# Kernel tuning notes

Hardware: AMD Instinct MI355X
Metric: run time of the kernel (lower is better)

Reference implementation:

```python
import jax, jax.numpy as jnp
import numpy as np

NUM_EMBEDDINGS = 512
EMBEDDING_DIM = 64
COMMITMENT_COST = 0.25


def setup_inputs() -> dict:
    key = jax.random.key(0)
    k1, k2 = jax.random.split(key)
    inputs = jax.random.normal(k1, (4, 64, 32, 32, 32), dtype=jnp.float32)
    # torch init: uniform(-1/K, 1/K)
    lim = 1.0 / NUM_EMBEDDINGS
    embedding = jax.random.uniform(k2, (NUM_EMBEDDINGS, EMBEDDING_DIM),
                                   dtype=jnp.float32, minval=-lim, maxval=lim)
    return {"inputs": inputs, "embedding": embedding}


def reference(inputs, embedding):
    # inputs: [B, C, D, H, W] with C == embedding_dim
    x = jnp.transpose(inputs, (0, 2, 3, 4, 1))            # [B,D,H,W,C]
    input_shape = x.shape
    flat = x.reshape(-1, EMBEDDING_DIM)                    # [N,C]
    # squared euclidean distances via matmul expansion
    d = (jnp.sum(flat ** 2, axis=1, keepdims=True)
         + jnp.sum(embedding ** 2, axis=1)
         - 2.0 * flat @ embedding.T)                       # [N,K]
    encoding_indices = jnp.argmin(d, axis=1)               # [N]
    quantized = embedding[encoding_indices].reshape(input_shape)  # [B,D,H,W,C]
    q_latent_loss = jnp.mean((jax.lax.stop_gradient(quantized) - x) ** 2)
    e_latent_loss = jnp.mean((quantized - jax.lax.stop_gradient(x)) ** 2)
    loss = q_latent_loss + COMMITMENT_COST * e_latent_loss
    # straight-through estimator
    quantized = x + jax.lax.stop_gradient(quantized - x)
    quantized = jnp.transpose(quantized, (0, 4, 1, 2, 3))  # [B,C,D,H,W]
    indices = encoding_indices.reshape(input_shape[:-1])   # [B,D,H,W]
    return quantized, loss, indices
```

## Files before the change

kernel.cpp:

```cpp
#include <hip/hip_runtime.h>
#include <math.h>

#define NROWS   131072
#define NCH     64
#define NEMB    512
#define CH_STRIDE 32768
#define B_STRIDE  (64*32768)
#define Q_ELEMS   8388608

#define NP_AVX512_SUM 1


__global__ __launch_bounds__(64)
void vq_esq(const float* __restrict__ emb, float* __restrict__ esq) {
    int k = blockIdx.x * 64 + threadIdx.x;
    if (k < NEMB) {
        const float* e = emb + k * NCH;
        float s = 0.f;
        #pragma unroll
        for (int c = 0; c < NCH; ++c) s = fmaf(e[c], e[c], s);
        esq[k] = s;
    }
}

__global__ __launch_bounds__(256)
void vq_main(const float* __restrict__ in, const float* __restrict__ emb,
             const float* __restrict__ esq,
             float* __restrict__ out_q, float* __restrict__ out_idx,
             double* __restrict__ loss_acc) {
    int n = blockIdx.x * 256 + threadIdx.x;
    int b = n >> 15;
    int s = n & 32767;
    const float* xin = in + b * B_STRIDE + s;

    float x[NCH];
    #pragma unroll
    for (int c = 0; c < NCH; ++c) x[c] = xin[c * CH_STRIDE];

    float A;
#if NP_AVX512_SUM
    {
        float L[16];
        #pragma unroll
        for (int i = 0; i < 16; ++i) {
            float q0 = x[i +  0] * x[i +  0];
            float q1 = x[i + 16] * x[i + 16];
            float q2 = x[i + 32] * x[i + 32];
            float q3 = x[i + 48] * x[i + 48];
            asm volatile("" : "+v"(q0), "+v"(q1), "+v"(q2), "+v"(q3));
            L[i] = (q0 + q1) + (q2 + q3);
        }
        float F[8];
        #pragma unroll
        for (int i = 0; i < 8; ++i) F[i] = L[i] + L[i + 8];
        float G[4];
        #pragma unroll
        for (int i = 0; i < 4; ++i) G[i] = F[i] + F[i + 4];
        float H0 = G[0] + G[2];
        float H1 = G[1] + G[3];
        A = H0 + H1;
    }
#else
    {
        float r[8];
        #pragma unroll
        for (int j = 0; j < 8; ++j) {
            float q = x[j] * x[j];
            asm volatile("" : "+v"(q));
            r[j] = q;
        }
        #pragma unroll
        for (int i = 8; i < 64; i += 8) {
            #pragma unroll
            for (int j = 0; j < 8; ++j) {
                float q = x[i + j] * x[i + j];
                asm volatile("" : "+v"(q));
                r[j] += q;
            }
        }
        A = ((r[0] + r[1]) + (r[2] + r[3])) + ((r[4] + r[5]) + (r[6] + r[7]));
    }
#endif

    #pragma unroll
    for (int c = 0; c < NCH; ++c) x[c] = x[c] + x[c];

    float m1 = 3.4e38f;
    int   i1 = 0;
    for (int k = 0; k < NEMB; ++k) {
        const float* e = emb + k * NCH;
        float acc = 0.f;
        #pragma unroll
        for (int c = 0; c < NCH; ++c) acc = fmaf(x[c], e[c], acc);
        float t1 = A + esq[k];
        float d  = t1 - acc;
        if (d < m1) { m1 = d; i1 = k; }
    }

    const float* q  = emb + i1 * NCH;
    float*       oq = out_q + b * B_STRIDE + s;
    double rl = 0.0;
    #pragma unroll
    for (int c = 0; c < NCH; ++c) {
        float qc = q[c];
        oq[c * CH_STRIDE] = qc;
        double dd = (double)qc - (double)(0.5f * x[c]);
        rl += dd * dd;
    }
    out_idx[n] = (float)i1;

    #pragma unroll
    for (int off = 32; off; off >>= 1) rl += __shfl_down(rl, off);
    if ((threadIdx.x & 63) == 0) atomicAdd(loss_acc, rl);
}

__global__ void vq_loss_final(const double* __restrict__ loss_acc,
                              float* __restrict__ out_loss) {
    if (threadIdx.x == 0)
        *out_loss = (float)((*loss_acc) * (1.25 / (double)Q_ELEMS));
}

extern "C" void kernel_launch(void* const* d_in, const int* in_sizes, int n_in,
                              void* d_out, int out_size, void* d_ws, size_t ws_size,
                              hipStream_t stream) {
    const float* in  = (const float*)d_in[0];
    const float* emb = (const float*)d_in[1];

    float* out_q    = (float*)d_out;
    float* out_loss = out_q + Q_ELEMS;
    float* out_idx  = out_q + Q_ELEMS + 1;

    char*   ws       = (char*)d_ws;
    double* loss_acc = (double*)ws;
    float*  esq      = (float*)(ws + 16);

    hipMemsetAsync(d_ws, 0, 16, stream);
    vq_esq<<<8, 64, 0, stream>>>(emb, esq);
    vq_main<<<NROWS / 256, 256, 0, stream>>>(in, emb, esq, out_q, out_idx,
                                             loss_acc);
    vq_loss_final<<<1, 64, 0, stream>>>(loss_acc, out_loss);
}
```

Before: 304.1 us.

## Split codebook scan across blocks and add separate argmin-finish kernel

The single fused kernel is split into two. The scan kernel divides the 512 codebook entries into 4 slices, one per block, and each block writes a packed (distance bits, index) partial minimum per row to workspace. A finish kernel takes the min of the 4 packed values, gathers the codeword with float4 loads, writes the outputs and accumulates the loss. This gives 4x more blocks to fill the GPU, which was launching only 512 blocks. The cost is reading the input 4 times in the scan, reading it again in the finish kernel, and the extra partials traffic.

After: 263.5 us. 13.3% less time.

```diff
diff --git a/kernel.cpp b/kernel.cpp
--- a/kernel.cpp
+++ b/kernel.cpp
@@ -7,8 +7,8 @@
 #define CH_STRIDE 32768
 #define B_STRIDE  (64*32768)
 #define Q_ELEMS   8388608
-
-#define NP_AVX512_SUM 1
+#define SPLITS  4
+#define KPQ     (NEMB/SPLITS)
 
 
 __global__ __launch_bounds__(64)
@@ -23,12 +23,13 @@
     }
 }
 
-__global__ __launch_bounds__(256)
-void vq_main(const float* __restrict__ in, const float* __restrict__ emb,
+__global__ __launch_bounds__(256, 4)
+void vq_scan(const float* __restrict__ in, const float* __restrict__ emb,
              const float* __restrict__ esq,
-             float* __restrict__ out_q, float* __restrict__ out_idx,
-             double* __restrict__ loss_acc) {
-    int n = blockIdx.x * 256 + threadIdx.x;
+             unsigned long long* __restrict__ parts) {
+    int q      = blockIdx.x & (SPLITS - 1);
+    int rowblk = blockIdx.x >> 2;
+    int n      = rowblk * 256 + threadIdx.x;
     int b = n >> 15;
     int s = n & 32767;
     const float* xin = in + b * B_STRIDE + s;
@@ -38,7 +39,6 @@
     for (int c = 0; c < NCH; ++c) x[c] = xin[c * CH_STRIDE];
 
     float A;
-#if NP_AVX512_SUM
     {
         float L[16];
         #pragma unroll
@@ -56,58 +56,69 @@
         float G[4];
         #pragma unroll
         for (int i = 0; i < 4; ++i) G[i] = F[i] + F[i + 4];
-        float H0 = G[0] + G[2];
-        float H1 = G[1] + G[3];
-        A = H0 + H1;
+        A = (G[0] + G[2]) + (G[1] + G[3]);
     }
-#else
-    {
-        float r[8];
-        #pragma unroll
-        for (int j = 0; j < 8; ++j) {
-            float q = x[j] * x[j];
-            asm volatile("" : "+v"(q));
-            r[j] = q;
-        }
-        #pragma unroll
-        for (int i = 8; i < 64; i += 8) {
-            #pragma unroll
-            for (int j = 0; j < 8; ++j) {
-                float q = x[i + j] * x[i + j];
-                asm volatile("" : "+v"(q));
-                r[j] += q;
-            }
-        }
-        A = ((r[0] + r[1]) + (r[2] + r[3])) + ((r[4] + r[5]) + (r[6] + r[7]));
-    }
-#endif
 
-    #pragma unroll
-    for (int c = 0; c < NCH; ++c) x[c] = x[c] + x[c];
-
+    int k0 = __builtin_amdgcn_readfirstlane(q * KPQ);
     float m1 = 3.4e38f;
-    int   i1 = 0;
-    for (int k = 0; k < NEMB; ++k) {
+    int   i1 = k0;
+    for (int j = 0; j < KPQ; ++j) {
+        int k = k0 + j;
         const float* e = emb + k * NCH;
         float acc = 0.f;
         #pragma unroll
         for (int c = 0; c < NCH; ++c) acc = fmaf(x[c], e[c], acc);
         float t1 = A + esq[k];
-        float d  = t1 - acc;
-        if (d < m1) { m1 = d; i1 = k; }
+        float d  = t1 - (acc + acc);
+        bool lt = d < m1;
+        m1 = lt ? d : m1;
+        i1 = lt ? k : i1;
     }
 
-    const float* q  = emb + i1 * NCH;
-    float*       oq = out_q + b * B_STRIDE + s;
+    unsigned long long pk =
+        ((unsigned long long)__float_as_uint(m1) << 32) | (unsigned)i1;
+    parts[(unsigned)n * SPLITS + q] = pk;
+}
+
+__global__ __launch_bounds__(256)
+void vq_finish(const float* __restrict__ in, const float* __restrict__ emb,
+               const unsigned long long* __restrict__ parts,
+               float* __restrict__ out_q, float* __restrict__ out_idx,
+               double* __restrict__ loss_acc) {
+    int n = blockIdx.x * 256 + threadIdx.x;
+    int b = n >> 15;
+    int s = n & 32767;
+
+    ulonglong2 pa = *reinterpret_cast<const ulonglong2*>(parts + (unsigned)n * 4);
+    ulonglong2 pb = *reinterpret_cast<const ulonglong2*>(parts + (unsigned)n * 4 + 2);
+    unsigned long long pk = pa.x;
+    if (pa.y < pk) pk = pa.y;
+    if (pb.x < pk) pk = pb.x;
+    if (pb.y < pk) pk = pb.y;
+    int w = (int)(pk & 0xFFFFu);
+
+    const float* xin = in + b * B_STRIDE + s;
+    const float* qr  = emb + w * NCH;
+    float*       oq  = out_q + b * B_STRIDE + s;
     double rl = 0.0;
     #pragma unroll
-    for (int c = 0; c < NCH; ++c) {
-        float qc = q[c];
-        oq[c * CH_STRIDE] = qc;
-        double dd = (double)qc - (double)(0.5f * x[c]);
-        rl += dd * dd;
+    for (int c = 0; c < NCH; c += 4) {
+        float4 qv = *reinterpret_cast<const float4*>(qr + c);
+        float x0 = xin[(c + 0) * CH_STRIDE];
+        float x1 = xin[(c + 1) * CH_STRIDE];
+        float x2 = xin[(c + 2) * CH_STRIDE];
+        float x3 = xin[(c + 3) * CH_STRIDE];
+        oq[(c + 0) * CH_STRIDE] = qv.x;
+        oq[(c + 1) * CH_STRIDE] = qv.y;
+        oq[(c + 2) * CH_STRIDE] = qv.z;
+        oq[(c + 3) * CH_STRIDE] = qv.w;
+        double d0 = (double)qv.x - (double)x0;
+        double d1 = (double)qv.y - (double)x1;
+        double d2 = (double)qv.z - (double)x2;
+        double d3 = (double)qv.w - (double)x3;
+        rl += d0 * d0 + d1 * d1 + d2 * d2 + d3 * d3;
     }
-    out_idx[n] = (float)i1;
+    out_idx[n] = (float)w;
 
     #pragma unroll
     for (int off = 32; off; off >>= 1) rl += __shfl_down(rl, off);
@@ -133,10 +144,12 @@
     char*   ws       = (char*)d_ws;
     double* loss_acc = (double*)ws;
     float*  esq      = (float*)(ws + 16);
+    unsigned long long* parts = (unsigned long long*)(ws + 4096);
 
     hipMemsetAsync(d_ws, 0, 16, stream);
     vq_esq<<<8, 64, 0, stream>>>(emb, esq);
-    vq_main<<<NROWS / 256, 256, 0, stream>>>(in, emb, esq, out_q, out_idx,
-                                             loss_acc);
+    vq_scan<<<(NROWS / 256) * SPLITS, 256, 0, stream>>>(in, emb, esq, parts);
+    vq_finish<<<NROWS / 256, 256, 0, stream>>>(in, emb, parts,
+                                               out_q, out_idx, loss_acc);
     vq_loss_final<<<1, 64, 0, stream>>>(loss_acc, out_loss);
 }
```
